# Kernel tuning notes

Measured on AMD Instinct MI355X. Metric: run time of the kernel, lower is better.

## Reference

```python
import math
import jax, jax.numpy as jnp
import numpy as np

S, B, IN, D, H, L, F, WIN = 500, 32, 256, 512, 8, 2, 2048, 100


def setup_inputs() -> dict:
    key = jax.random.key(0)
    ks = jax.random.split(key, 20)
    s = 0.02
    inp = {
        "x": jax.random.normal(ks[0], (S, B, IN), dtype=jnp.float32),
        "W_emb": jax.random.normal(ks[1], (IN, D), dtype=jnp.float32) * s,
        "b_emb": jnp.zeros((D,), jnp.float32),
        "Wq": jax.random.normal(ks[2], (L, D, D), dtype=jnp.float32) * s,
        "bq": jnp.zeros((L, D), jnp.float32),
        "Wk": jax.random.normal(ks[3], (L, D, D), dtype=jnp.float32) * s,
        "bk": jnp.zeros((L, D), jnp.float32),
        "Wv": jax.random.normal(ks[4], (L, D, D), dtype=jnp.float32) * s,
        "bv": jnp.zeros((L, D), jnp.float32),
        "Wo": jax.random.normal(ks[5], (L, D, D), dtype=jnp.float32) * s,
        "bo": jnp.zeros((L, D), jnp.float32),
        "ln1_s": jnp.ones((L, D), jnp.float32),
        "ln1_b": jnp.zeros((L, D), jnp.float32),
        "W1": jax.random.normal(ks[6], (L, D, F), dtype=jnp.float32) * s,
        "b1": jnp.zeros((L, F), jnp.float32),
        "W2": jax.random.normal(ks[7], (L, F, D), dtype=jnp.float32) * s,
        "b2": jnp.zeros((L, D), jnp.float32),
        "ln2_s": jnp.ones((L, D), jnp.float32),
        "ln2_b": jnp.zeros((L, D), jnp.float32),
    }
    return inp


def _pos_encoding(seq_len, d_model, dtype):
    pos = jnp.arange(seq_len, dtype=dtype)[:, None]
    div = jnp.exp(jnp.arange(0, d_model, 2, dtype=dtype) * (-math.log(10000.0) / d_model))
    ang = pos * div  # [S, D/2]
    # interleave sin/cos -> pe[:,0::2]=sin, pe[:,1::2]=cos
    return jnp.stack([jnp.sin(ang), jnp.cos(ang)], axis=-1).reshape(seq_len, d_model)


def _layernorm(y, scale, bias, eps=1e-5):
    m = y.mean(-1, keepdims=True)
    v = ((y - m) ** 2).mean(-1, keepdims=True)
    return (y - m) / jnp.sqrt(v + eps) * scale + bias


def reference(x, W_emb, b_emb, Wq, bq, Wk, bk, Wv, bv, Wo, bo,
              ln1_s, ln1_b, W1, b1, W2, b2, ln2_s, ln2_b):
    seq_len, batch, _ = x.shape
    d_model = W_emb.shape[1]
    n_layers = Wq.shape[0]
    hd = d_model // H

    # embedding + positional encoding (dropout is identity in eval mode)
    h = x @ W_emb + b_emb + _pos_encoding(seq_len, d_model, x.dtype)[:, None, :]

    idx = jnp.arange(seq_len)
    diff = idx[:, None] - idx[None, :]
    amask = jnp.where((diff >= 0) & (diff < WIN), 0.0, -jnp.inf).astype(x.dtype)

    for l in range(n_layers):
        # multi-head self-attention (post-norm encoder layer)
        q = (h @ Wq[l] + bq[l]).reshape(seq_len, batch, H, hd)
        k = (h @ Wk[l] + bk[l]).reshape(seq_len, batch, H, hd)
        v = (h @ Wv[l] + bv[l]).reshape(seq_len, batch, H, hd)
        scores = jnp.einsum('ibhd,jbhd->bhij', q, k) / math.sqrt(hd) + amask
        attn = jax.nn.softmax(scores, axis=-1)
        o = jnp.einsum('bhij,jbhd->ibhd', attn, v).reshape(seq_len, batch, d_model)
        h = _layernorm(h + o @ Wo[l] + bo[l], ln1_s[l], ln1_b[l])
        # feed-forward (relu)
        ff = jax.nn.relu(h @ W1[l] + b1[l]) @ W2[l] + b2[l]
        h = _layernorm(h + ff, ln2_s[l], ln2_b[l])
    return h
```

## Files before the change

kernel.cpp:

```cpp
#include <hip/hip_runtime.h>
#include <stdint.h>

#define SEQ   500
#define BATCH 32
#define DIN   256
#define DM    512
#define NH    8
#define NL    2
#define DF    2048
#define WINSZ 100
#define HD    64
#define ROWS  (SEQ*BATCH)
#define MPAD  16128

typedef __bf16 bf16x8 __attribute__((ext_vector_type(8)));
typedef float  f32x4  __attribute__((ext_vector_type(4)));

__device__ __forceinline__ unsigned short bfbits(float f) {
    unsigned int u = __builtin_bit_cast(unsigned int, f);
    u = u + 0x7fffu + ((u >> 16) & 1u);
    return (unsigned short)(u >> 16);
}
__device__ __forceinline__ unsigned int pack2(float a, float b) {
    return (unsigned int)bfbits(a) | ((unsigned int)bfbits(b) << 16);
}
__device__ __forceinline__ float blo(unsigned int u) { return __builtin_bit_cast(float, u << 16); }
__device__ __forceinline__ float bhi(unsigned int u) { return __builtin_bit_cast(float, u & 0xffff0000u); }

__device__ __forceinline__ void async16(void* lds, const void* g) {
    __builtin_amdgcn_global_load_lds((__attribute__((address_space(1))) void*)(void*)g,
                                     (__attribute__((address_space(3))) void*)(void*)lds,
                                     16, 0, 0);
}

__global__ __launch_bounds__(256) void wprep_k(const float* __restrict__ Wemb,
                                               const float* __restrict__ Wq,
                                               const float* __restrict__ Wk,
                                               const float* __restrict__ Wv,
                                               const float* __restrict__ Wo,
                                               const float* __restrict__ W1,
                                               const float* __restrict__ W2,
                                               unsigned short* __restrict__ wt_emb,
                                               unsigned short* __restrict__ wt_qkv,
                                               unsigned short* __restrict__ wt_o,
                                               unsigned short* __restrict__ wt_1,
                                               unsigned short* __restrict__ wt_2) {
    __shared__ float t[32][33];
    const int tile = blockIdx.x;
    const float* src;
    unsigned short* dst;
    int R, C, bx, by;
    if (tile < 128) {
        src = Wemb; dst = wt_emb; R = DIN; C = DM;
        bx = tile & 15; by = tile >> 4;
    } else if (tile < 128 + 2048) {
        int u = tile - 128;
        int m = u >> 8, local = u & 255;
        int l = m >> 2, w = m & 3;
        src = ((w == 0) ? Wq : (w == 1) ? Wk : (w == 2) ? Wv : Wo) + (size_t)l * DM * DM;
        dst = (w < 3) ? wt_qkv + (size_t)l * 3 * DM * DM + (size_t)w * DM * DM
                      : wt_o + (size_t)l * DM * DM;
        R = DM; C = DM;
        bx = local & 15; by = local >> 4;
    } else if (tile < 128 + 2048 + 2048) {
        int u = tile - (128 + 2048);
        int l = u >> 10, local = u & 1023;
        src = W1 + (size_t)l * DM * DF; dst = wt_1 + (size_t)l * DF * DM;
        R = DM; C = DF;
        bx = local & 63; by = local >> 6;
    } else {
        int u = tile - (128 + 2048 + 2048);
        int l = u >> 10, local = u & 1023;
        src = W2 + (size_t)l * DF * DM; dst = wt_2 + (size_t)l * DM * DF;
        R = DF; C = DM;
        bx = local & 15; by = local >> 4;
    }
    const int c0 = bx * 32, r0 = by * 32;
    const int tx = threadIdx.x, ty = threadIdx.y;
#pragma unroll
    for (int k = 0; k < 32; k += 8)
        t[ty + k][tx] = src[(size_t)(r0 + ty + k) * C + c0 + tx];
    __syncthreads();
#pragma unroll
    for (int k = 0; k < 32; k += 8)
        dst[(size_t)(c0 + ty + k) * R + r0 + tx] = bfbits(t[tx][ty + k]);
}

__global__ __launch_bounds__(256) void prep_k(const float* __restrict__ bq,
                                              const float* __restrict__ bk,
                                              const float* __restrict__ bv,
                                              float* __restrict__ bias_qkv,
                                              float* __restrict__ pe) {
    int tid = blockIdx.x * 256 + threadIdx.x;
    if (tid < SEQ * DM) {
        int s = tid >> 9, c = tid & 511;
        int p = c >> 1;
        float div = expf(-(float)(2 * p) * (9.210340371976184f / 512.0f));
        float ang = (float)s * div;
        pe[tid] = (c & 1) ? cosf(ang) : sinf(ang);
    }
    if (tid < NL * 3 * DM) {
        int l = tid / (3 * DM), r = tid % (3 * DM);
        float v = (r < DM) ? bq[l * DM + r]
                : (r < 2 * DM) ? bk[l * DM + r - DM]
                               : bv[l * DM + r - 2 * DM];
        bias_qkv[tid] = v;
    }
}

__global__ __launch_bounds__(256) void xcast_k(const float* __restrict__ x,
                                               unsigned short* __restrict__ xb, int n) {
    int i = (blockIdx.x * 256 + threadIdx.x) * 4;
    if (i < n) {
        float4 v = *(const float4*)&x[i];
        uint2 o; o.x = pack2(v.x, v.y); o.y = pack2(v.z, v.w);
        *(uint2*)&xb[i] = o;
    }
}

template <int BM, int BN, int MODE>
__global__ __launch_bounds__(256, 2)
void gemm2_k(const unsigned short* __restrict__ A,
             const unsigned short* __restrict__ Wt,
             const float* __restrict__ bias,
             unsigned short* __restrict__ outB,
             const float* __restrict__ pe,
             int Mt, int Nt, int K, int N) {
    constexpr int NTH = 256;
    constexpr int SLOTS = 3;
    constexpr int PD  = 2;
    constexpr int NWC = BN / 64;
    constexpr int MI  = 4;
    constexpr int JSH = 5;

    __shared__ unsigned short LA[SLOTS][BM * 32];
    __shared__ unsigned short LB[SLOTS][BN * 32];

    const int tid = threadIdx.x, lane = tid & 63, wid = tid >> 6;
    const int wr = wid / NWC, wc = wid % NWC;
    const int lr = lane & 15, grp = lane >> 4;

    int lin = blockIdx.x;
    int base_m = (lin / (8 * Nt)) * 8;
    int Gc = min(8, Mt - base_m);
    int rem = lin - base_m * Nt;
    int mt = base_m + rem % Gc, nt = rem / Gc;
    const int m0 = mt * BM, n0 = nt * BN;

    const int NKT = K >> 5;

    auto stageA = [&](int kt, int part) {
        int slot = kt % SLOTS, k0 = kt << 5;
        int g = part * NTH + tid;
        int row = g >> 2, c = g & 3;
        int src = c ^ ((row >> 1) & 3);
        async16(&LA[slot][g * 8], A + (size_t)(m0 + row) * K + k0 + src * 8);
    };
    auto stageB = [&](int kt, int part) {
        int slot = kt % SLOTS, k0 = kt << 5;
        int g = part * NTH + tid;
        int pos = g >> 2, cs = g & 3;
        int j   = pos >> JSH;
        int wcc = (pos >> 4) & (NWC - 1);
        int lrr = pos & 15;
        int rb  = wcc * 64 + lrr * 4 + j;
        int c   = cs ^ ((rb >> 3) & 3);
        async16(&LB[slot][g * 8], Wt + (size_t)(n0 + rb) * K + k0 + c * 8);
    };

    f32x4 acc[MI][4] = {};

#pragma unroll
    for (int t = 0; t < PD; ++t) {
        stageA(t, 0); stageA(t, 1); stageB(t, 0); stageB(t, 1);
    }

    for (int kt = 0; kt < NKT; ++kt) {
        const int slot = kt % SLOTS;
        const bool pf = (kt + PD < NKT);
        if (kt + 1 < NKT)      asm volatile("s_waitcnt vmcnt(4)" ::: "memory");
        else                   asm volatile("s_waitcnt vmcnt(0)" ::: "memory");
        __builtin_amdgcn_s_barrier();
        __builtin_amdgcn_sched_barrier(0);

        const int bxor = grp ^ ((lr >> 1) & 3);
        bf16x8 af[MI], bf[4];

#pragma unroll
        for (int i = 0; i < MI; ++i) {
            int ra = wr * (MI * 16) + i * 16 + lr;
            af[i] = *(const bf16x8*)&LA[slot][ra * 32 + ((grp ^ ((ra >> 1) & 3)) << 3)];
        }
#pragma unroll
        for (int j = 0; j < 2; ++j) {
            int pos = j * (16 * NWC) + wc * 16 + lr;
            bf[j] = *(const bf16x8*)&LB[slot][(pos * 4 + bxor) * 8];
        }
        if (pf) { stageA(kt + PD, 0); stageA(kt + PD, 1); }
        __builtin_amdgcn_s_setprio(1);
#pragma unroll
        for (int i = 0; i < MI; ++i)
#pragma unroll
            for (int j = 0; j < 2; ++j)
                acc[i][j] = __builtin_amdgcn_mfma_f32_16x16x32_bf16(af[i], bf[j], acc[i][j], 0, 0, 0);
        __builtin_amdgcn_s_setprio(0);
        __builtin_amdgcn_s_barrier();
        __builtin_amdgcn_sched_barrier(0);

#pragma unroll
        for (int j = 2; j < 4; ++j) {
            int pos = j * (16 * NWC) + wc * 16 + lr;
            bf[j] = *(const bf16x8*)&LB[slot][(pos * 4 + bxor) * 8];
        }
        if (pf) { stageB(kt + PD, 0); stageB(kt + PD, 1); }
        __builtin_amdgcn_s_setprio(1);
#pragma unroll
        for (int i = 0; i < MI; ++i)
#pragma unroll
            for (int j = 2; j < 4; ++j)
                acc[i][j] = __builtin_amdgcn_mfma_f32_16x16x32_bf16(af[i], bf[j], acc[i][j], 0, 0, 0);
        __builtin_amdgcn_s_setprio(0);
        __builtin_amdgcn_s_barrier();
        __builtin_amdgcn_sched_barrier(0);
    }

    const int colb = n0 + wc * 64 + lr * 4;
    float4 bv4 = *(const float4*)&bias[colb];
#pragma unroll
    for (int i = 0; i < MI; ++i) {
#pragma unroll
        for (int v = 0; v < 4; ++v) {
            int row = m0 + wr * (MI * 16) + i * 16 + grp * 4 + v;
            float f0 = acc[i][0][v] + bv4.x;
            float f1 = acc[i][1][v] + bv4.y;
            float f2 = acc[i][2][v] + bv4.z;
            float f3 = acc[i][3][v] + bv4.w;
            if (MODE == 2) {
                f0 = fmaxf(f0, 0.f); f1 = fmaxf(f1, 0.f);
                f2 = fmaxf(f2, 0.f); f3 = fmaxf(f3, 0.f);
            }
            if (MODE == 3) {
                int s = min(row >> 5, SEQ - 1);
                float4 p4 = *(const float4*)&pe[(size_t)s * DM + colb];
                f0 += p4.x; f1 += p4.y; f2 += p4.z; f3 += p4.w;
            }
            uint2 wv; wv.x = pack2(f0, f1); wv.y = pack2(f2, f3);
            *(uint2*)&outB[(size_t)row * N + colb] = wv;
        }
    }
}

template <int MODE>
__global__ __launch_bounds__(512, 2)
void gemm3_k(const unsigned short* __restrict__ A,
             const unsigned short* __restrict__ Wt,
             const float* __restrict__ bias,
             unsigned short* __restrict__ outB,
             int Mt, int Nt, int K, int N) {
    __shared__ unsigned short LA[2][256 * 64];
    __shared__ unsigned short LB[2][256 * 64];

    const int tid = threadIdx.x, lane = tid & 63, wid = tid >> 6;
    const int wr = wid >> 2, wc = wid & 3;
    const int lr = lane & 15, grp = lane >> 4;

    int lin = blockIdx.x;
    int base_m = (lin / (8 * Nt)) * 8;
    int Gc = min(8, Mt - base_m);
    int rem = lin - base_m * Nt;
    int mt = base_m + rem % Gc, nt = rem / Gc;
    const int m0 = mt * 256, n0 = nt * 256;

    const int NKT = K >> 6;

    auto stA = [&](int kt, int part) {
        int slot = kt & 1, k0 = kt << 6;
        int g = part * 512 + tid;
        int row = g >> 3, c = g & 7;
        int src = c ^ (row & 7);
        async16(&LA[slot][g * 8], A + (size_t)(m0 + row) * K + k0 + src * 8);
    };
    auto stB = [&](int kt, int part) {
        int slot = kt & 1, k0 = kt << 6;
        int g = part * 512 + tid;
        int pos = g >> 3, cs = g & 7;
        int j = pos >> 6, wcc = (pos >> 4) & 3, lrr = pos & 15;
        int rb = wcc * 64 + lrr * 4 + j;
        int c = cs ^ (lrr & 7);
        async16(&LB[slot][g * 8], Wt + (size_t)(n0 + rb) * K + k0 + c * 8);
    };

    f32x4 acc[8][4] = {};

    stB(0, 0); stB(0, 1); stA(0, 0); stA(0, 2); stB(0, 2); stB(0, 3); stA(0, 1); stA(0, 3);

    for (int kt = 0; kt < NKT; ++kt) {
        const int slot = kt & 1;
        const bool pf = (kt + 1 < NKT);
        bf16x8 afL[8], afH[8], bf01[4], bf23[4];

        asm volatile("s_waitcnt vmcnt(4)" ::: "memory");
        __builtin_amdgcn_s_barrier();
        __builtin_amdgcn_sched_barrier(0);
#pragma unroll
        for (int j = 0; j < 2; ++j)
#pragma unroll
            for (int kk = 0; kk < 2; ++kk) {
                int pos = j * 64 + wc * 16 + lr;
                bf01[j * 2 + kk] = *(const bf16x8*)&LB[slot][pos * 64 + (((kk * 4 + grp) ^ (lr & 7)) << 3)];
            }
#pragma unroll
        for (int i = 0; i < 4; ++i)
#pragma unroll
            for (int kk = 0; kk < 2; ++kk) {
                int ra = wr * 128 + i * 16 + lr;
                afL[i * 2 + kk] = *(const bf16x8*)&LA[slot][ra * 64 + (((kk * 4 + grp) ^ (ra & 7)) << 3)];
            }
        if (pf) { stB(kt + 1, 0); stB(kt + 1, 1); }
        __builtin_amdgcn_s_setprio(1);
#pragma unroll
        for (int i = 0; i < 4; ++i)
#pragma unroll
            for (int j = 0; j < 2; ++j)
#pragma unroll
                for (int kk = 0; kk < 2; ++kk)
                    acc[i][j] = __builtin_amdgcn_mfma_f32_16x16x32_bf16(afL[i * 2 + kk], bf01[j * 2 + kk], acc[i][j], 0, 0, 0);
        __builtin_amdgcn_s_setprio(0);
        __builtin_amdgcn_sched_barrier(0);

        if (pf) asm volatile("s_waitcnt vmcnt(4)" ::: "memory");
        else    asm volatile("s_waitcnt vmcnt(2)" ::: "memory");
        __builtin_amdgcn_s_barrier();
        __builtin_amdgcn_sched_barrier(0);
#pragma unroll
        for (int j = 0; j < 2; ++j)
#pragma unroll
            for (int kk = 0; kk < 2; ++kk) {
                int pos = (2 + j) * 64 + wc * 16 + lr;
                bf23[j * 2 + kk] = *(const bf16x8*)&LB[slot][pos * 64 + (((kk * 4 + grp) ^ (lr & 7)) << 3)];
            }
        if (pf) { stA(kt + 1, 0); stA(kt + 1, 2); }
        __builtin_amdgcn_s_setprio(1);
#pragma unroll
        for (int i = 0; i < 4; ++i)
#pragma unroll
            for (int j = 0; j < 2; ++j)
#pragma unroll
                for (int kk = 0; kk < 2; ++kk)
                    acc[i][2 + j] = __builtin_amdgcn_mfma_f32_16x16x32_bf16(afL[i * 2 + kk], bf23[j * 2 + kk], acc[i][2 + j], 0, 0, 0);
        __builtin_amdgcn_s_setprio(0);
        __builtin_amdgcn_sched_barrier(0);

        if (pf) asm volatile("s_waitcnt vmcnt(4)" ::: "memory");
        else    asm volatile("s_waitcnt vmcnt(0)" ::: "memory");
        __builtin_amdgcn_s_barrier();
        __builtin_amdgcn_sched_barrier(0);
#pragma unroll
        for (int i = 0; i < 4; ++i)
#pragma unroll
            for (int kk = 0; kk < 2; ++kk) {
                int ra = wr * 128 + (4 + i) * 16 + lr;
                afH[i * 2 + kk] = *(const bf16x8*)&LA[slot][ra * 64 + (((kk * 4 + grp) ^ (ra & 7)) << 3)];
            }
        if (pf) { stB(kt + 1, 2); stB(kt + 1, 3); }
        __builtin_amdgcn_s_setprio(1);
#pragma unroll
        for (int i = 0; i < 4; ++i)
#pragma unroll
            for (int j = 0; j < 2; ++j)
#pragma unroll
                for (int kk = 0; kk < 2; ++kk)
                    acc[4 + i][j] = __builtin_amdgcn_mfma_f32_16x16x32_bf16(afH[i * 2 + kk], bf01[j * 2 + kk], acc[4 + i][j], 0, 0, 0);
        __builtin_amdgcn_s_setprio(0);
        __builtin_amdgcn_sched_barrier(0);

        __builtin_amdgcn_s_barrier();
        __builtin_amdgcn_sched_barrier(0);
        if (pf) { stA(kt + 1, 1); stA(kt + 1, 3); }
        __builtin_amdgcn_s_setprio(1);
#pragma unroll
        for (int i = 0; i < 4; ++i)
#pragma unroll
            for (int j = 0; j < 2; ++j)
#pragma unroll
                for (int kk = 0; kk < 2; ++kk)
                    acc[4 + i][2 + j] = __builtin_amdgcn_mfma_f32_16x16x32_bf16(afH[i * 2 + kk], bf23[j * 2 + kk], acc[4 + i][2 + j], 0, 0, 0);
        __builtin_amdgcn_s_setprio(0);
        __builtin_amdgcn_sched_barrier(0);
    }

    const int colb = n0 + wc * 64 + lr * 4;
    float4 bv4 = *(const float4*)&bias[colb];
#pragma unroll
    for (int i = 0; i < 8; ++i) {
#pragma unroll
        for (int v = 0; v < 4; ++v) {
            int row = m0 + wr * 128 + i * 16 + grp * 4 + v;
            float f0 = acc[i][0][v] + bv4.x;
            float f1 = acc[i][1][v] + bv4.y;
            float f2 = acc[i][2][v] + bv4.z;
            float f3 = acc[i][3][v] + bv4.w;
            if (MODE == 2) {
                f0 = fmaxf(f0, 0.f); f1 = fmaxf(f1, 0.f);
                f2 = fmaxf(f2, 0.f); f3 = fmaxf(f3, 0.f);
            }
            uint2 wv; wv.x = pack2(f0, f1); wv.y = pack2(f2, f3);
            *(uint2*)&outB[(size_t)row * N + colb] = wv;
        }
    }
}

__global__ __launch_bounds__(256) void vtrans_k(const unsigned short* __restrict__ qkv,
                                                unsigned short* __restrict__ vT) {
    __shared__ unsigned short t[32][72];
    const int s0 = blockIdx.x * 32;
    const int bh = blockIdx.y;
    const int b = bh >> 3, h = bh & 7;
    const int tid = threadIdx.x;
    {
        int sl = tid >> 3;
        int c  = tid & 7;
        int s  = s0 + sl;
        uint4 val = {0, 0, 0, 0};
        if (s < SEQ)
            val = *(const uint4*)&qkv[(size_t)(s * BATCH + b) * (3 * DM) + 2 * DM + h * HD + c * 8];
        *(uint4*)&t[sl][c * 8] = val;
    }
    __syncthreads();
    {
        int d  = tid >> 2;
        int s8 = (tid & 3) * 8;
        unsigned short v[8];
#pragma unroll
        for (int j = 0; j < 8; ++j) v[j] = t[s8 + j][d];
        *(uint4*)&vT[(size_t)(bh * 64 + d) * 512 + s0 + s8] = *(uint4*)v;
    }
}

#define QBLK  64
#define NIB   8
#define KTIL  11
#define KSTR  72
#define VSTR  200
#define PSTR  200

__global__ __launch_bounds__(256, 3) void attn_k(const unsigned short* __restrict__ qkv,
                                                 const unsigned short* __restrict__ vT,
                                                 unsigned short* __restrict__ ob) {
    __shared__ unsigned short KV[12800];
    __shared__ unsigned short Pl[64 * PSTR];

    const int ib = blockIdx.x & (NIB - 1), bh = blockIdx.x >> 3;
    const int b = bh >> 3, h = bh & 7;
    const int i0 = ib * QBLK;
    const int jbase = max(0, i0 - (WINSZ - 1));
    const int jend  = min(SEQ - 1, i0 + QBLK - 1);
    const int nkeys = jend - jbase + 1;
    const int NT  = (nkeys + 15) >> 4;
    const int NKS = (nkeys + 31) >> 5;
    const int tid = threadIdx.x, lane = tid & 63, w = tid >> 6;
    const int q15 = lane & 15, grp = lane >> 4;

#pragma unroll
    for (int it = 0; it < 6; ++it) {
        int g = it * 256 + tid;
        if (g < nkeys * 8) {
            int row = g >> 3, c = g & 7;
            uint4 val = *(const uint4*)&qkv[(size_t)((jbase + row) * BATCH + b) * (3 * DM)
                                            + DM + h * HD + c * 8];
            *(uint4*)&KV[row * KSTR + c * 8] = val;
        }
    }
    uint4 vreg[6];
#pragma unroll
    for (int it = 0; it < 6; ++it) {
        int g = it * 256 + tid;
        int r = g / 24, c = g - r * 24;
        uint4 val = {0, 0, 0, 0};
        if (c * 8 < nkeys && jbase + c * 8 + 8 <= 512)
            val = *(const uint4*)&vT[(size_t)(bh * 64 + r) * 512 + jbase + c * 8];
        vreg[it] = val;
    }
    bf16x8 qav, qbv;
    {
        int iq = min(i0 + w * 16 + q15, SEQ - 1);
        size_t qrow = (size_t)(iq * BATCH + b) * (3 * DM) + h * HD;
        uint4 a = *(const uint4*)&qkv[qrow + grp * 8];
        uint4 c = *(const uint4*)&qkv[qrow + 32 + grp * 8];
        qav = __builtin_bit_cast(bf16x8, a);
        qbv = __builtin_bit_cast(bf16x8, c);
    }
    __syncthreads();

    const int i = i0 + w * 16 + q15;
    float sc[KTIL][4];
#pragma unroll
    for (int t = 0; t < KTIL; ++t) {
        if (t >= NT) continue;
        f32x4 acc = {};
        int row = t * 16 + q15;
        bf16x8 kf0 = *(const bf16x8*)&KV[row * KSTR + grp * 8];
        acc = __builtin_amdgcn_mfma_f32_16x16x32_bf16(kf0, qav, acc, 0, 0, 0);
        bf16x8 kf1 = *(const bf16x8*)&KV[row * KSTR + 32 + grp * 8];
        acc = __builtin_amdgcn_mfma_f32_16x16x32_bf16(kf1, qbv, acc, 0, 0, 0);
#pragma unroll
        for (int v = 0; v < 4; ++v) {
            int key = jbase + t * 16 + grp * 4 + v;
            bool valid = (key <= i) && (key > i - WINSZ);
            sc[t][v] = valid ? acc[v] * 0.125f : -1e30f;
        }
    }
    float m = -1e30f;
#pragma unroll
    for (int t = 0; t < KTIL; ++t) {
        if (t >= NT) continue;
#pragma unroll
        for (int v = 0; v < 4; ++v) m = fmaxf(m, sc[t][v]);
    }
    m = fmaxf(m, __shfl_xor(m, 16));
    m = fmaxf(m, __shfl_xor(m, 32));
    float sum = 0.f;
#pragma unroll
    for (int t = 0; t < KTIL; ++t) {
        if (t >= NT) continue;
#pragma unroll
        for (int v = 0; v < 4; ++v) {
            float p = __expf(sc[t][v] - m);
            sc[t][v] = p;
            sum += p;
        }
    }
    sum += __shfl_xor(sum, 16);
    sum += __shfl_xor(sum, 32);

    __syncthreads();

#pragma unroll
    for (int it = 0; it < 6; ++it) {
        int g = it * 256 + tid;
        int r = g / 24, c = g - r * 24;
        *(uint4*)&KV[r * VSTR + c * 8] = vreg[it];
    }
#pragma unroll
    for (int t = 0; t < KTIL; ++t) {
        if (t >= NT) continue;
        uint2 pk;
        pk.x = pack2(sc[t][0], sc[t][1]);
        pk.y = pack2(sc[t][2], sc[t][3]);
        *(uint2*)&Pl[(w * 16 + q15) * PSTR + t * 16 + grp * 4] = pk;
    }
    if (NT * 16 < NKS * 32) {
        uint2 z = {0, 0};
        *(uint2*)&Pl[(w * 16 + q15) * PSTR + NT * 16 + grp * 4] = z;
    }
    __syncthreads();

    f32x4 oacc[4] = {};
#pragma unroll
    for (int ks = 0; ks < 6; ++ks) {
        if (ks >= NKS) continue;
        bf16x8 pf = *(const bf16x8*)&Pl[(w * 16 + q15) * PSTR + ks * 32 + grp * 8];
#pragma unroll
        for (int dt = 0; dt < 4; ++dt) {
            bf16x8 vf = *(const bf16x8*)&KV[(dt * 16 + q15) * VSTR + ks * 32 + grp * 8];
            oacc[dt] = __builtin_amdgcn_mfma_f32_16x16x32_bf16(pf, vf, oacc[dt], 0, 0, 0);
        }
    }

#pragma unroll
    for (int v = 0; v < 4; ++v) {
        float rsv = 1.0f / __shfl(sum, grp * 4 + v);
        int irow = i0 + w * 16 + grp * 4 + v;
        if (irow < SEQ) {
            size_t base = (size_t)(irow * BATCH + b) * DM + h * HD + q15;
#pragma unroll
            for (int dt = 0; dt < 4; ++dt)
                ob[base + dt * 16] = bfbits(oacc[dt][v] * rsv);
        }
    }
}

template <int FOUT>
__global__ __launch_bounds__(256) void ln_k(const unsigned short* __restrict__ hin,
                                            const unsigned short* __restrict__ yin,
                                            const float* __restrict__ sc,
                                            const float* __restrict__ bi,
                                            unsigned short* __restrict__ hb,
                                            float* __restrict__ fout) {
    int row = blockIdx.x * 4 + (threadIdx.x >> 6);
    int lane = threadIdx.x & 63;
    size_t base = (size_t)row * DM + lane * 8;
    uint4 hw = *(const uint4*)&hin[base];
    uint4 yw = *(const uint4*)&yin[base];
    float x[8] = {blo(hw.x) + blo(yw.x), bhi(hw.x) + bhi(yw.x),
                  blo(hw.y) + blo(yw.y), bhi(hw.y) + bhi(yw.y),
                  blo(hw.z) + blo(yw.z), bhi(hw.z) + bhi(yw.z),
                  blo(hw.w) + blo(yw.w), bhi(hw.w) + bhi(yw.w)};
    float s = 0.f;
#pragma unroll
    for (int k = 0; k < 8; ++k) s += x[k];
#pragma unroll
    for (int off = 32; off; off >>= 1) s += __shfl_xor(s, off);
    float mean = s * (1.f / DM);
    float q = 0.f;
#pragma unroll
    for (int k = 0; k < 8; ++k) { float d = x[k] - mean; q = fmaf(d, d, q); }
#pragma unroll
    for (int off = 32; off; off >>= 1) q += __shfl_xor(q, off);
    float rstd = rsqrtf(q * (1.f / DM) + 1e-5f);
    float4 s0 = *(const float4*)&sc[lane * 8], s1 = *(const float4*)&sc[lane * 8 + 4];
    float4 b0 = *(const float4*)&bi[lane * 8], b1 = *(const float4*)&bi[lane * 8 + 4];
    float o[8];
    o[0] = (x[0] - mean) * rstd * s0.x + b0.x;  o[1] = (x[1] - mean) * rstd * s0.y + b0.y;
    o[2] = (x[2] - mean) * rstd * s0.z + b0.z;  o[3] = (x[3] - mean) * rstd * s0.w + b0.w;
    o[4] = (x[4] - mean) * rstd * s1.x + b1.x;  o[5] = (x[5] - mean) * rstd * s1.y + b1.y;
    o[6] = (x[6] - mean) * rstd * s1.z + b1.z;  o[7] = (x[7] - mean) * rstd * s1.w + b1.w;
    if (FOUT) {
        float4 w0 = {o[0], o[1], o[2], o[3]}, w1 = {o[4], o[5], o[6], o[7]};
        *(float4*)&fout[base] = w0;
        *(float4*)&fout[base + 4] = w1;
    } else {
        uint4 pk = {pack2(o[0], o[1]), pack2(o[2], o[3]), pack2(o[4], o[5]), pack2(o[6], o[7])};
        *(uint4*)&hb[base] = pk;
    }
}

extern "C" void kernel_launch(void* const* d_in, const int* in_sizes, int n_in,
                              void* d_out, int out_size, void* d_ws, size_t ws_size,
                              hipStream_t stream) {
    const float* x     = (const float*)d_in[0];
    const float* Wemb  = (const float*)d_in[1];
    const float* bemb  = (const float*)d_in[2];
    const float* Wq    = (const float*)d_in[3];
    const float* bq    = (const float*)d_in[4];
    const float* Wk    = (const float*)d_in[5];
    const float* bk    = (const float*)d_in[6];
    const float* Wv    = (const float*)d_in[7];
    const float* bv    = (const float*)d_in[8];
    const float* Wo    = (const float*)d_in[9];
    const float* bo    = (const float*)d_in[10];
    const float* ln1s  = (const float*)d_in[11];
    const float* ln1b  = (const float*)d_in[12];
    const float* W1    = (const float*)d_in[13];
    const float* b1    = (const float*)d_in[14];
    const float* W2    = (const float*)d_in[15];
    const float* b2    = (const float*)d_in[16];
    const float* ln2s  = (const float*)d_in[17];
    const float* ln2b  = (const float*)d_in[18];

    char* p = (char*)d_ws;
    auto carve = [&](size_t bytes) { char* r = p; p += (bytes + 255) & ~(size_t)255; return r; };

    unsigned short* wt_emb = (unsigned short*)carve((size_t)DM * DIN * 2);
    unsigned short* wt_qkv = (unsigned short*)carve((size_t)NL * 3 * DM * DM * 2);
    unsigned short* wt_o   = (unsigned short*)carve((size_t)NL * DM * DM * 2);
    unsigned short* wt_1   = (unsigned short*)carve((size_t)NL * DF * DM * 2);
    unsigned short* wt_2   = (unsigned short*)carve((size_t)NL * DM * DF * 2);
    float*          biasq  = (float*)carve((size_t)NL * 3 * DM * 4);
    float*          pe     = (float*)carve((size_t)SEQ * DM * 4);
    unsigned short* xb     = (unsigned short*)carve((size_t)MPAD * DIN * 2);
    unsigned short* h      = (unsigned short*)carve((size_t)MPAD * DM * 2);
    unsigned short* ob     = (unsigned short*)carve((size_t)MPAD * DM * 2);
    unsigned short* t0b    = (unsigned short*)carve((size_t)MPAD * DM * 2);
    unsigned short* vT     = (unsigned short*)carve((size_t)BATCH * NH * 64 * 512 * 2 + 1024);
    unsigned short* qkv    = (unsigned short*)carve((size_t)MPAD * DF * 2);
    unsigned short* f1     = qkv;

    dim3 blk256(256);

    wprep_k<<<dim3(6272), dim3(32, 8), 0, stream>>>(Wemb, Wq, Wk, Wv, Wo, W1, W2,
                                                    wt_emb, wt_qkv, wt_o, wt_1, wt_2);
    prep_k<<<dim3((SEQ * DM + 255) / 256), blk256, 0, stream>>>(bq, bk, bv, biasq, pe);
    xcast_k<<<dim3(ROWS * DIN / 4 / 256), blk256, 0, stream>>>(x, xb, ROWS * DIN);

    const int Mt256 = MPAD / 256;
    const int Mt128 = MPAD / 128;

    gemm2_k<128, 128, 3><<<dim3(Mt128 * 4), blk256, 0, stream>>>(
        xb, wt_emb, bemb, h, pe, Mt128, 4, DIN, DM);

    for (int l = 0; l < NL; ++l) {
        gemm2_k<128, 128, 1><<<dim3(Mt128 * 12), blk256, 0, stream>>>(
            h, wt_qkv + (size_t)l * 3 * DM * DM, biasq + (size_t)l * 3 * DM,
            qkv, nullptr, Mt128, 12, DM, 3 * DM);
        vtrans_k<<<dim3(16, BATCH * NH), blk256, 0, stream>>>(qkv, vT);
        attn_k<<<dim3(BATCH * NH * NIB), blk256, 0, stream>>>(qkv, vT, ob);
        gemm2_k<128, 128, 1><<<dim3(Mt128 * 4), blk256, 0, stream>>>(
            ob, wt_o + (size_t)l * DM * DM, bo + (size_t)l * DM,
            t0b, nullptr, Mt128, 4, DM, DM);
        ln_k<0><<<dim3(ROWS / 4), blk256, 0, stream>>>(h, t0b, ln1s + (size_t)l * DM, ln1b + (size_t)l * DM, h, nullptr);
        gemm3_k<2><<<dim3(Mt256 * 8), dim3(512), 0, stream>>>(
            h, wt_1 + (size_t)l * DF * DM, b1 + (size_t)l * DF,
            f1, Mt256, 8, DM, DF);
        gemm2_k<128, 128, 1><<<dim3(Mt128 * 4), blk256, 0, stream>>>(
            f1, wt_2 + (size_t)l * DM * DF, b2 + (size_t)l * DM,
            t0b, nullptr, Mt128, 4, DF, DM);
        if (l == NL - 1)
            ln_k<1><<<dim3(ROWS / 4), blk256, 0, stream>>>(h, t0b, ln2s + (size_t)l * DM, ln2b + (size_t)l * DM, nullptr, (float*)d_out);
        else
            ln_k<0><<<dim3(ROWS / 4), blk256, 0, stream>>>(h, t0b, ln2s + (size_t)l * DM, ln2b + (size_t)l * DM, h, nullptr);
    }
}
```

Baseline: 392.8 us.

## Use split-K large-tile GEMM for output and FFN2 projections, reduce in LayerNorm

Replaces the 128x128 GEMM for the attention-output and second FFN projections with the 256x256 gemm3 kernel split into two K halves. Each half writes a separate bf16 partial result, and the LayerNorm kernel sums both partials plus the bias before normalizing. This is meant to raise the per-block arithmetic intensity and keep the grid filled despite N=512. It costs an extra partial buffer write/read, and summing bf16-rounded partials adds some rounding error.

```diff
diff --git a/kernel.cpp b/kernel.cpp
--- a/kernel.cpp
+++ b/kernel.cpp
@@ -255,8 +255,9 @@
 void gemm3_k(const unsigned short* __restrict__ A,
              const unsigned short* __restrict__ Wt,
              const float* __restrict__ bias,
-             unsigned short* __restrict__ outB,
-             int Mt, int Nt, int K, int N) {
+             unsigned short* __restrict__ out0,
+             unsigned short* __restrict__ out1,
+             int Mt, int Nt, int Ksub, int Kfull, int N) {
     __shared__ unsigned short LA[2][256 * 64];
     __shared__ unsigned short LB[2][256 * 64];
 
@@ -264,30 +265,34 @@
     const int wr = wid >> 2, wc = wid & 3;
     const int lr = lane & 15, grp = lane >> 4;
 
-    int lin = blockIdx.x;
+    const int mn = Mt * Nt;
+    const int kh = blockIdx.x / mn;
+    int lin = blockIdx.x % mn;
     int base_m = (lin / (8 * Nt)) * 8;
     int Gc = min(8, Mt - base_m);
     int rem = lin - base_m * Nt;
     int mt = base_m + rem % Gc, nt = rem / Gc;
     const int m0 = mt * 256, n0 = nt * 256;
-
-    const int NKT = K >> 6;
+    const int kbase = kh * Ksub;
+    unsigned short* outp = kh ? out1 : out0;
+
+    const int NKT = Ksub >> 6;
 
     auto stA = [&](int kt, int part) {
-        int slot = kt & 1, k0 = kt << 6;
+        int slot = kt & 1, k0 = kbase + (kt << 6);
         int g = part * 512 + tid;
         int row = g >> 3, c = g & 7;
         int src = c ^ (row & 7);
-        async16(&LA[slot][g * 8], A + (size_t)(m0 + row) * K + k0 + src * 8);
+        async16(&LA[slot][g * 8], A + (size_t)(m0 + row) * Kfull + k0 + src * 8);
     };
     auto stB = [&](int kt, int part) {
-        int slot = kt & 1, k0 = kt << 6;
+        int slot = kt & 1, k0 = kbase + (kt << 6);
         int g = part * 512 + tid;
         int pos = g >> 3, cs = g & 7;
         int j = pos >> 6, wcc = (pos >> 4) & 3, lrr = pos & 15;
         int rb = wcc * 64 + lrr * 4 + j;
         int c = cs ^ (lrr & 7);
-        async16(&LB[slot][g * 8], Wt + (size_t)(n0 + rb) * K + k0 + c * 8);
+        async16(&LB[slot][g * 8], Wt + (size_t)(n0 + rb) * Kfull + k0 + c * 8);
     };
 
     f32x4 acc[8][4] = {};
@@ -390,7 +395,8 @@
     }
 
     const int colb = n0 + wc * 64 + lr * 4;
-    float4 bv4 = *(const float4*)&bias[colb];
+    float4 bv4 = {0.f, 0.f, 0.f, 0.f};
+    if constexpr (MODE != 0) bv4 = *(const float4*)&bias[colb];
 #pragma unroll
     for (int i = 0; i < 8; ++i) {
 #pragma unroll
@@ -405,7 +411,7 @@
                 f2 = fmaxf(f2, 0.f); f3 = fmaxf(f3, 0.f);
             }
             uint2 wv; wv.x = pack2(f0, f1); wv.y = pack2(f2, f3);
-            *(uint2*)&outB[(size_t)row * N + colb] = wv;
+            *(uint2*)&outp[(size_t)row * N + colb] = wv;
         }
     }
 }
@@ -582,7 +588,9 @@
 
 template <int FOUT>
 __global__ __launch_bounds__(256) void ln_k(const unsigned short* __restrict__ hin,
-                                            const unsigned short* __restrict__ yin,
+                                            const unsigned short* __restrict__ y0,
+                                            const unsigned short* __restrict__ y1,
+                                            const float* __restrict__ bvec,
                                             const float* __restrict__ sc,
                                             const float* __restrict__ bi,
                                             unsigned short* __restrict__ hb,
@@ -591,11 +599,17 @@
     int lane = threadIdx.x & 63;
     size_t base = (size_t)row * DM + lane * 8;
     uint4 hw = *(const uint4*)&hin[base];
-    uint4 yw = *(const uint4*)&yin[base];
-    float x[8] = {blo(hw.x) + blo(yw.x), bhi(hw.x) + bhi(yw.x),
-                  blo(hw.y) + blo(yw.y), bhi(hw.y) + bhi(yw.y),
-                  blo(hw.z) + blo(yw.z), bhi(hw.z) + bhi(yw.z),
-                  blo(hw.w) + blo(yw.w), bhi(hw.w) + bhi(yw.w)};
+    uint4 ya = *(const uint4*)&y0[base];
+    uint4 yb = *(const uint4*)&y1[base];
+    float4 bv0 = *(const float4*)&bvec[lane * 8], bv1 = *(const float4*)&bvec[lane * 8 + 4];
+    float x[8] = {blo(hw.x) + blo(ya.x) + blo(yb.x) + bv0.x,
+                  bhi(hw.x) + bhi(ya.x) + bhi(yb.x) + bv0.y,
+                  blo(hw.y) + blo(ya.y) + blo(yb.y) + bv0.z,
+                  bhi(hw.y) + bhi(ya.y) + bhi(yb.y) + bv0.w,
+                  blo(hw.z) + blo(ya.z) + blo(yb.z) + bv1.x,
+                  bhi(hw.z) + bhi(ya.z) + bhi(yb.z) + bv1.y,
+                  blo(hw.w) + blo(ya.w) + blo(yb.w) + bv1.z,
+                  bhi(hw.w) + bhi(ya.w) + bhi(yb.w) + bv1.w};
     float s = 0.f;
 #pragma unroll
     for (int k = 0; k < 8; ++k) s += x[k];
@@ -662,6 +676,7 @@
     unsigned short* h      = (unsigned short*)carve((size_t)MPAD * DM * 2);
     unsigned short* ob     = (unsigned short*)carve((size_t)MPAD * DM * 2);
     unsigned short* t0b    = (unsigned short*)carve((size_t)MPAD * DM * 2);
+    unsigned short* t0c    = (unsigned short*)carve((size_t)MPAD * DM * 2);
     unsigned short* vT     = (unsigned short*)carve((size_t)BATCH * NH * 64 * 512 * 2 + 1024);
     unsigned short* qkv    = (unsigned short*)carve((size_t)MPAD * DF * 2);
     unsigned short* f1     = qkv;
@@ -685,19 +700,25 @@
             qkv, nullptr, Mt128, 12, DM, 3 * DM);
         vtrans_k<<<dim3(16, BATCH * NH), blk256, 0, stream>>>(qkv, vT);
         attn_k<<<dim3(BATCH * NH * NIB), blk256, 0, stream>>>(qkv, vT, ob);
-        gemm2_k<128, 128, 1><<<dim3(Mt128 * 4), blk256, 0, stream>>>(
-            ob, wt_o + (size_t)l * DM * DM, bo + (size_t)l * DM,
-            t0b, nullptr, Mt128, 4, DM, DM);
-        ln_k<0><<<dim3(ROWS / 4), blk256, 0, stream>>>(h, t0b, ln1s + (size_t)l * DM, ln1b + (size_t)l * DM, h, nullptr);
+        gemm3_k<0><<<dim3(Mt256 * 2 * 2), dim3(512), 0, stream>>>(
+            ob, wt_o + (size_t)l * DM * DM, nullptr,
+            t0b, t0c, Mt256, 2, 256, DM, DM);
+        ln_k<0><<<dim3(ROWS / 4), blk256, 0, stream>>>(
+            h, t0b, t0c, bo + (size_t)l * DM,
+            ln1s + (size_t)l * DM, ln1b + (size_t)l * DM, h, nullptr);
         gemm3_k<2><<<dim3(Mt256 * 8), dim3(512), 0, stream>>>(
             h, wt_1 + (size_t)l * DF * DM, b1 + (size_t)l * DF,
-            f1, Mt256, 8, DM, DF);
-        gemm2_k<128, 128, 1><<<dim3(Mt128 * 4), blk256, 0, stream>>>(
-            f1, wt_2 + (size_t)l * DM * DF, b2 + (size_t)l * DM,
-            t0b, nullptr, Mt128, 4, DF, DM);
+            f1, nullptr, Mt256, 8, DM, DM, DF);
+        gemm3_k<0><<<dim3(Mt256 * 2 * 2), dim3(512), 0, stream>>>(
+            f1, wt_2 + (size_t)l * DM * DF, nullptr,
+            t0b, t0c, Mt256, 2, 1024, DF, DM);
         if (l == NL - 1)
-            ln_k<1><<<dim3(ROWS / 4), blk256, 0, stream>>>(h, t0b, ln2s + (size_t)l * DM, ln2b + (size_t)l * DM, nullptr, (float*)d_out);
+            ln_k<1><<<dim3(ROWS / 4), blk256, 0, stream>>>(
+                h, t0b, t0c, b2 + (size_t)l * DM,
+                ln2s + (size_t)l * DM, ln2b + (size_t)l * DM, nullptr, (float*)d_out);
         else
-            ln_k<0><<<dim3(ROWS / 4), blk256, 0, stream>>>(h, t0b, ln2s + (size_t)l * DM, ln2b + (size_t)l * DM, h, nullptr);
-    }
-}
+            ln_k<0><<<dim3(ROWS / 4), blk256, 0, stream>>>(
+                h, t0b, t0c, b2 + (size_t)l * DM,
+                ln2s + (size_t)l * DM, ln2b + (size_t)l * DM, h, nullptr);
+    }
+}
```

Measured after the change: 388.3 us (median of 2 runs). No clear change (-1.2%).
